# Performance work log

Measured on AMD Instinct MI355X. Metric: run time of the kernel, lower is better.

Reference implementation:

```python
import jax, jax.numpy as jnp
import numpy as np

NUM_CLASSES = 20
NUM_ANC = 5
S_ = 1 + NUM_CLASSES                   # 21
GDIM = 1 + NUM_CLASSES + 4 + 1 + 4     # 30: conf, cls20, txywh4, weight, gltrb4
ANCS_SCALE = np.array([[0.05, 0.07], [0.12, 0.15], [0.25, 0.30], [0.45, 0.55], [0.75, 0.80]], dtype=np.float32)
LOSS_W_CLS = 1.0
EPS16 = 0.0009765625  # torch.finfo(torch.float16).eps
BATCH, GRID, NBOX = 64, 38, 16
C_IN = (S_ + 4) * NUM_ANC              # 125


def ltrb2xywh(b):
    return jnp.concatenate([(b[..., :2] + b[..., 2:]) * 0.5, b[..., 2:] - b[..., :2]], -1)


def x_bce(p, g):
    p = jnp.clip(p, EPS16, 1.0 - EPS16)
    return -(g * jnp.log(p) + (1.0 - g) * jnp.log(1.0 - p))


def match_one(gboxes, glabels, ancs, grid):
    # gboxes [N,4] ltrb in [0,1]; glabels [N] in [1,NUM_CLASSES]
    xywh = ltrb2xywh(gboxes)
    cxy, wh = xywh[:, :2], xywh[:, 2:]
    # IoU between co-centered GT wh and anchor wh (both centered at origin)
    inter = jnp.minimum(wh[:, None, 0], ancs[None, :, 0]) * jnp.minimum(wh[:, None, 1], ancs[None, :, 1])
    union = (wh[:, 0] * wh[:, 1])[:, None] + (ancs[:, 0] * ancs[:, 1])[None, :] - inter
    ids_p = jnp.argmax(inter / union, axis=-1)                           # [N] best anchor per GT
    colrow = jnp.clip(jnp.floor(cxy * grid).astype(jnp.int32), 0, grid - 1)
    txy = cxy * grid - colrow.astype(cxy.dtype)                          # cell-relative offset
    twh = jnp.log(wh / ancs[ids_p])                                      # log wh ratio vs matched anchor
    weight = 2.0 - wh[:, 0] * wh[:, 1]
    onehot = jax.nn.one_hot(glabels - 1, NUM_CLASSES, dtype=gboxes.dtype)
    ones = jnp.ones((gboxes.shape[0], 1), gboxes.dtype)
    tvec = jnp.concatenate([ones, onehot, txy, twh, weight[:, None], gboxes], -1)  # [N,GDIM]
    g = jnp.zeros((grid, grid, NUM_ANC, GDIM), gboxes.dtype)
    col, row = colrow[:, 0], colrow[:, 1]
    g = g.at[row, col, :, 0].set(-1.0)       # mark all anchors at GT cell as ignore
    g = g.at[row, col, ids_p].set(tvec)      # matched anchor gets full target (conf=1)
    return g


def _loss(pyolos, gboxes_ltrb, glabels):
    batch, c, h, w = pyolos.shape
    p = pyolos.reshape(batch, S_ + 4, NUM_ANC, h * w)
    p = p.transpose(0, 3, 2, 1).reshape(batch, -1, S_ + 4)               # [B, h*w*A, 25]
    ancs = jnp.asarray(ANCS_SCALE)
    gy = jax.vmap(lambda b, l: match_one(b, l, ancs, h))(gboxes_ltrb, glabels)
    gy = gy.reshape(batch, -1, GDIM)                                     # [B, h*w*A, 30]
    gconf = gy[:, :, 0]
    mask_pos = gconf > 0
    mask_neg = gconf == 0
    nums_pos = jnp.clip(mask_pos.sum(-1).astype(jnp.float32), EPS16)
    nums_neg = jnp.clip(mask_neg.sum(-1).astype(jnp.float32), EPS16)
    mpf = mask_pos.astype(p.dtype)
    n_pos_tot = jnp.maximum(mpf.sum(), 1.0)
    # ---- cls loss over positives (masked mean == .mean() over selected) ----
    pcls = jax.nn.sigmoid(p[:, :, 1:S_])
    l_cls = (x_bce(pcls, gy[:, :, 1:S_]).sum(-1) * mpf).sum() / n_pos_tot * LOSS_W_CLS
    # ---- conf focal loss (alpha=0.5, gamma=2), replicating sum(-1).sum(-1)/nums then mean ----
    pconf = jnp.clip(jax.nn.sigmoid(p[:, :, 0]), EPS16, 1.0 - EPS16)
    l_pos = -0.5 * (1.0 - pconf) ** 2 * jnp.log(pconf) * gconf * mpf
    l_neg = -0.5 * pconf ** 2 * jnp.log(1.0 - pconf) * (1.0 - gconf) * mask_neg.astype(p.dtype)
    l_conf_pos = (l_pos.sum() / nums_pos).mean()
    l_conf_neg = (l_neg.sum() / nums_neg).mean() * 3.0
    # ---- box loss (MODE_TRAIN != 4 branch). NB: original indexes weight at S_+4+1 ----
    pxy = jax.nn.sigmoid(p[:, :, S_:S_ + 2])
    pwh = p[:, :, S_ + 2:S_ + 4]
    w_pos = gy[:, :, S_ + 4 + 1]
    l_txty = ((x_bce(pxy, gy[:, :, S_:S_ + 2]).sum(-1) * w_pos) * mpf).sum() / n_pos_tot
    l_twth = ((((pwh - gy[:, :, S_ + 2:S_ + 4]) ** 2).sum(-1) * w_pos) * mpf).sum() / n_pos_tot
    return l_conf_pos + l_conf_neg + l_cls + l_txty + l_twth


def setup_inputs():
    key = jax.random.key(0)
    k1, k2, k3, k4 = jax.random.split(key, 4)
    pyolos = jax.random.normal(k1, (BATCH, C_IN, GRID, GRID), jnp.float32)
    cxy = jax.random.uniform(k2, (BATCH, NBOX, 2), jnp.float32, 0.1, 0.9)
    wh = jax.random.uniform(k3, (BATCH, NBOX, 2), jnp.float32, 0.05, 0.3)
    gboxes_ltrb = jnp.concatenate([cxy - wh * 0.5, cxy + wh * 0.5], -1)
    glabels = jax.random.randint(k4, (BATCH, NBOX), 1, NUM_CLASSES + 1)
    return {"pyolos": pyolos, "gboxes_ltrb": gboxes_ltrb, "glabels": glabels}


def reference(pyolos, gboxes_ltrb, glabels):
    return _loss(pyolos, gboxes_ltrb, glabels)
```

## Files before the change

### kernel.cpp

```cpp
#include <hip/hip_runtime.h>

#define BATCH 64
#define GRIDW 38
#define HW 1444
#define NBOX 16
#define NANC 5
#define NCLS 20
#define SLOTS 7220
#define CIN 125
#define EPSC 0.0009765625f
#define BPB 29
#define NBLK (BATCH * BPB)
#define PSTRIDE 7

struct BoxRec {
  int   cell;
  int   ids;
  int   lab;
  float tx, ty, tw, th;
  float wleft;
};

__constant__ float ANCW[5] = {0.05f, 0.12f, 0.25f, 0.45f, 0.75f};
__constant__ float ANCH[5] = {0.07f, 0.15f, 0.30f, 0.55f, 0.80f};

__global__ void __launch_bounds__(256) main_kernel(
    const float* __restrict__ pyolos,
    const float* __restrict__ gboxes,
    const int* __restrict__ glabels,
    float* __restrict__ partials) {
  int b     = blockIdx.x / BPB;
  int chunk = blockIdx.x - b * BPB;

  __shared__ BoxRec sbox[NBOX];
  if (threadIdx.x < NBOX) {
    int n = threadIdx.x;
    const float* gb = gboxes + ((size_t)b * NBOX + n) * 4;
    float l  = gb[0], t = gb[1], r = gb[2], bt = gb[3];
    float cx = (l + r) * 0.5f, cy = (t + bt) * 0.5f;
    float w  = r - l,          h  = bt - t;
    int best = 0; float bestv = -1.0f;
    #pragma unroll
    for (int a = 0; a < NANC; ++a) {
      float inter = fminf(w, ANCW[a]) * fminf(h, ANCH[a]);
      float uni   = w * h + ANCW[a] * ANCH[a] - inter;
      float iou   = inter / uni;
      if (iou > bestv) { bestv = iou; best = a; }
    }
    int col = (int)floorf(cx * (float)GRIDW);
    int row = (int)floorf(cy * (float)GRIDW);
    col = min(max(col, 0), GRIDW - 1);
    row = min(max(row, 0), GRIDW - 1);
    BoxRec rec;
    rec.cell  = row * GRIDW + col;
    rec.ids   = best;
    rec.lab   = glabels[(size_t)b * NBOX + n] - 1;
    rec.tx    = cx * (float)GRIDW - (float)col;
    rec.ty    = cy * (float)GRIDW - (float)row;
    rec.tw    = logf(w / ANCW[best]);
    rec.th    = logf(h / ANCH[best]);
    rec.wleft = l;
    sbox[n] = rec;
  }
  __syncthreads();

  float s_pos = 0.f, s_neg = 0.f, s_cls = 0.f, s_txty = 0.f, s_twth = 0.f;
  float c_pos = 0.f, c_ign = 0.f;

  int sIdx = chunk * 256 + threadIdx.x;
  if (sIdx < SLOTS) {
    int j = sIdx / HW;
    int k = sIdx - j * HW;

    int posbox = -1; bool cellmatch = false;
    #pragma unroll
    for (int n = 0; n < NBOX; ++n) {
      if (sbox[n].cell == k) {
        cellmatch = true;
        if (sbox[n].ids == j) posbox = n;
      }
    }

    const float* pb = pyolos + (size_t)b * CIN * HW + k;
    float pconf = 1.0f / (1.0f + expf(-pb[(size_t)j * HW]));
    pconf = fminf(fmaxf(pconf, EPSC), 1.0f - EPSC);

    if (posbox >= 0) {
      c_pos = 1.f;
      float om = 1.0f - pconf;
      s_pos = -0.5f * om * om * logf(pconf);
      BoxRec rec = sbox[posbox];
      float csum = 0.f;
      for (int c = 0; c < NCLS; ++c) {
        float pc = 1.0f / (1.0f + expf(-pb[(size_t)((1 + c) * NANC + j) * HW]));
        pc = fminf(fmaxf(pc, EPSC), 1.0f - EPSC);
        csum += (c == rec.lab) ? -logf(pc) : -logf(1.0f - pc);
      }
      s_cls = csum;
      float px = 1.0f / (1.0f + expf(-pb[(size_t)(21 * NANC + j) * HW]));
      float py = 1.0f / (1.0f + expf(-pb[(size_t)(22 * NANC + j) * HW]));
      px = fminf(fmaxf(px, EPSC), 1.0f - EPSC);
      py = fminf(fmaxf(py, EPSC), 1.0f - EPSC);
      float bx = -(rec.tx * logf(px) + (1.0f - rec.tx) * logf(1.0f - px));
      float by = -(rec.ty * logf(py) + (1.0f - rec.ty) * logf(1.0f - py));
      s_txty = (bx + by) * rec.wleft;
      float pw = pb[(size_t)(23 * NANC + j) * HW];
      float ph = pb[(size_t)(24 * NANC + j) * HW];
      float dw = pw - rec.tw, dh = ph - rec.th;
      s_twth = (dw * dw + dh * dh) * rec.wleft;
    } else if (cellmatch) {
      c_ign = 1.f;
    } else {
      s_neg = -0.5f * pconf * pconf * logf(1.0f - pconf);
    }
  }

  __shared__ float red[4][PSTRIDE];
  int lane = threadIdx.x & 63;
  int wid  = threadIdx.x >> 6;
  for (int off = 32; off; off >>= 1) {
    s_pos  += __shfl_down(s_pos,  off, 64);
    s_neg  += __shfl_down(s_neg,  off, 64);
    s_cls  += __shfl_down(s_cls,  off, 64);
    s_txty += __shfl_down(s_txty, off, 64);
    s_twth += __shfl_down(s_twth, off, 64);
    c_pos  += __shfl_down(c_pos,  off, 64);
    c_ign  += __shfl_down(c_ign,  off, 64);
  }
  if (lane == 0) {
    red[wid][0] = s_pos;  red[wid][1] = s_neg; red[wid][2] = s_cls;
    red[wid][3] = s_txty; red[wid][4] = s_twth;
    red[wid][5] = c_pos;  red[wid][6] = c_ign;
  }
  __syncthreads();
  if (threadIdx.x == 0) {
    float a[PSTRIDE] = {0, 0, 0, 0, 0, 0, 0};
    for (int w2 = 0; w2 < 4; ++w2)
      for (int q = 0; q < PSTRIDE; ++q) a[q] += red[w2][q];
    float* mine = partials + (size_t)blockIdx.x * PSTRIDE;
    for (int q = 0; q < PSTRIDE; ++q) mine[q] = a[q];
  }
}

__global__ void finalize_kernel(const float* __restrict__ partials,
                                float* __restrict__ out) {
  double a[5] = {0, 0, 0, 0, 0};
  for (int i = threadIdx.x; i < NBLK; i += 256) {
    const float* p = partials + (size_t)i * PSTRIDE;
    a[0] += p[0]; a[1] += p[1]; a[2] += p[2]; a[3] += p[3]; a[4] += p[4];
  }
  __shared__ double redd[4][5];
  int lane = threadIdx.x & 63;
  int wid  = threadIdx.x >> 6;
  for (int off = 32; off; off >>= 1)
    for (int q = 0; q < 5; ++q) a[q] += __shfl_down(a[q], off, 64);
  if (lane == 0)
    for (int q = 0; q < 5; ++q) redd[wid][q] = a[q];

  double inv_pos = 0, inv_neg = 0, npos = 0;
  if (threadIdx.x < BATCH) {
    float p = 0.f, g = 0.f;
    const float* pp = partials + (size_t)threadIdx.x * BPB * PSTRIDE;
    for (int i = 0; i < BPB; ++i) { p += pp[i * PSTRIDE + 5]; g += pp[i * PSTRIDE + 6]; }
    double posf = (double)p;
    double negf = (double)SLOTS - (double)p - (double)g;
    inv_pos = 1.0 / fmax(posf, (double)EPSC);
    inv_neg = 1.0 / fmax(negf, (double)EPSC);
    npos = posf;
  }
  for (int off = 32; off; off >>= 1) {
    inv_pos += __shfl_down(inv_pos, off, 64);
    inv_neg += __shfl_down(inv_neg, off, 64);
    npos    += __shfl_down(npos,    off, 64);
  }
  __syncthreads();
  if (threadIdx.x == 0) {
    double s[5] = {0, 0, 0, 0, 0};
    for (int w2 = 0; w2 < 4; ++w2)
      for (int q = 0; q < 5; ++q) s[q] += redd[w2][q];
    double n_pos_tot = fmax(npos, 1.0);
    double loss = s[0] * (inv_pos / (double)BATCH)
                + 3.0 * s[1] * (inv_neg / (double)BATCH)
                + s[2] / n_pos_tot
                + s[3] / n_pos_tot
                + s[4] / n_pos_tot;
    out[0] = (float)loss;
  }
}

extern "C" void kernel_launch(void* const* d_in, const int* in_sizes, int n_in,
                              void* d_out, int out_size, void* d_ws, size_t ws_size,
                              hipStream_t stream) {
  const float* pyolos  = (const float*)d_in[0];
  const float* gboxes  = (const float*)d_in[1];
  const int*   glabels = (const int*)d_in[2];
  float* out = (float*)d_out;

  float* partials = (float*)d_ws;

  main_kernel<<<NBLK, 256, 0, stream>>>(pyolos, gboxes, glabels, partials);
  finalize_kernel<<<1, 256, 0, stream>>>(partials, out);
}
```

Baseline: 96.75 us.

## Fuse finalize into main kernel with one block per batch and flag-based last-block reduction

Merges the two-kernel reduce-then-finalize into a single launch. Each batch image is now handled by one block that loops over all anchor slots, writes per-batch partials including the inverse positive and negative counts, and publishes a release flag. The last block spins on the other blocks' flags and computes the final loss. This removes a kernel launch and the per-block partial scan, but cuts the grid from about 1856 blocks to 64, which lowers parallelism on a large GPU. It also relies on all blocks being co-resident and on flags that are never reset, so later calls may read stale state.

```diff
diff --git a/kernel.cpp b/kernel.cpp
--- a/kernel.cpp
+++ b/kernel.cpp
@@ -9,9 +9,8 @@
 #define SLOTS 7220
 #define CIN 125
 #define EPSC 0.0009765625f
-#define BPB 29
-#define NBLK (BATCH * BPB)
-#define PSTRIDE 7
+#define PSTRIDE 8
+#define MAGIC 0x5EEDFACEu
 
 struct BoxRec {
   int   cell;
@@ -24,13 +23,14 @@
 __constant__ float ANCW[5] = {0.05f, 0.12f, 0.25f, 0.45f, 0.75f};
 __constant__ float ANCH[5] = {0.07f, 0.15f, 0.30f, 0.55f, 0.80f};
 
-__global__ void __launch_bounds__(256) main_kernel(
+__global__ void __launch_bounds__(256) fused_kernel(
     const float* __restrict__ pyolos,
     const float* __restrict__ gboxes,
     const int* __restrict__ glabels,
-    float* __restrict__ partials) {
-  int b     = blockIdx.x / BPB;
-  int chunk = blockIdx.x - b * BPB;
+    float* __restrict__ partials,
+    unsigned int* __restrict__ flags,
+    float* __restrict__ out) {
+  int b = blockIdx.x;
 
   __shared__ BoxRec sbox[NBOX];
   if (threadIdx.x < NBOX) {
@@ -67,8 +67,8 @@
   float s_pos = 0.f, s_neg = 0.f, s_cls = 0.f, s_txty = 0.f, s_twth = 0.f;
   float c_pos = 0.f, c_ign = 0.f;
 
-  int sIdx = chunk * 256 + threadIdx.x;
-  if (sIdx < SLOTS) {
+  const float* pbase = pyolos + (size_t)b * CIN * HW;
+  for (int sIdx = threadIdx.x; sIdx < SLOTS; sIdx += 256) {
     int j = sIdx / HW;
     int k = sIdx - j * HW;
 
@@ -81,14 +81,14 @@
       }
     }
 
-    const float* pb = pyolos + (size_t)b * CIN * HW + k;
+    const float* pb = pbase + k;
     float pconf = 1.0f / (1.0f + expf(-pb[(size_t)j * HW]));
     pconf = fminf(fmaxf(pconf, EPSC), 1.0f - EPSC);
 
     if (posbox >= 0) {
-      c_pos = 1.f;
+      c_pos += 1.f;
       float om = 1.0f - pconf;
-      s_pos = -0.5f * om * om * logf(pconf);
+      s_pos += -0.5f * om * om * logf(pconf);
       BoxRec rec = sbox[posbox];
       float csum = 0.f;
       for (int c = 0; c < NCLS; ++c) {
@@ -96,26 +96,26 @@
         pc = fminf(fmaxf(pc, EPSC), 1.0f - EPSC);
         csum += (c == rec.lab) ? -logf(pc) : -logf(1.0f - pc);
       }
-      s_cls = csum;
+      s_cls += csum;
       float px = 1.0f / (1.0f + expf(-pb[(size_t)(21 * NANC + j) * HW]));
       float py = 1.0f / (1.0f + expf(-pb[(size_t)(22 * NANC + j) * HW]));
       px = fminf(fmaxf(px, EPSC), 1.0f - EPSC);
       py = fminf(fmaxf(py, EPSC), 1.0f - EPSC);
       float bx = -(rec.tx * logf(px) + (1.0f - rec.tx) * logf(1.0f - px));
       float by = -(rec.ty * logf(py) + (1.0f - rec.ty) * logf(1.0f - py));
-      s_txty = (bx + by) * rec.wleft;
+      s_txty += (bx + by) * rec.wleft;
       float pw = pb[(size_t)(23 * NANC + j) * HW];
       float ph = pb[(size_t)(24 * NANC + j) * HW];
       float dw = pw - rec.tw, dh = ph - rec.th;
-      s_twth = (dw * dw + dh * dh) * rec.wleft;
+      s_twth += (dw * dw + dh * dh) * rec.wleft;
     } else if (cellmatch) {
-      c_ign = 1.f;
+      c_ign += 1.f;
     } else {
-      s_neg = -0.5f * pconf * pconf * logf(1.0f - pconf);
-    }
-  }
-
-  __shared__ float red[4][PSTRIDE];
+      s_neg += -0.5f * pconf * pconf * logf(1.0f - pconf);
+    }
+  }
+
+  __shared__ float red[4][7];
   int lane = threadIdx.x & 63;
   int wid  = threadIdx.x >> 6;
   for (int off = 32; off; off >>= 1) {
@@ -133,58 +133,54 @@
     red[wid][5] = c_pos;  red[wid][6] = c_ign;
   }
   __syncthreads();
+
   if (threadIdx.x == 0) {
-    float a[PSTRIDE] = {0, 0, 0, 0, 0, 0, 0};
+    float a[7] = {0, 0, 0, 0, 0, 0, 0};
     for (int w2 = 0; w2 < 4; ++w2)
-      for (int q = 0; q < PSTRIDE; ++q) a[q] += red[w2][q];
-    float* mine = partials + (size_t)blockIdx.x * PSTRIDE;
-    for (int q = 0; q < PSTRIDE; ++q) mine[q] = a[q];
-  }
-}
-
-__global__ void finalize_kernel(const float* __restrict__ partials,
-                                float* __restrict__ out) {
-  double a[5] = {0, 0, 0, 0, 0};
-  for (int i = threadIdx.x; i < NBLK; i += 256) {
-    const float* p = partials + (size_t)i * PSTRIDE;
-    a[0] += p[0]; a[1] += p[1]; a[2] += p[2]; a[3] += p[3]; a[4] += p[4];
-  }
-  __shared__ double redd[4][5];
-  int lane = threadIdx.x & 63;
-  int wid  = threadIdx.x >> 6;
-  for (int off = 32; off; off >>= 1)
-    for (int q = 0; q < 5; ++q) a[q] += __shfl_down(a[q], off, 64);
-  if (lane == 0)
-    for (int q = 0; q < 5; ++q) redd[wid][q] = a[q];
-
-  double inv_pos = 0, inv_neg = 0, npos = 0;
-  if (threadIdx.x < BATCH) {
-    float p = 0.f, g = 0.f;
-    const float* pp = partials + (size_t)threadIdx.x * BPB * PSTRIDE;
-    for (int i = 0; i < BPB; ++i) { p += pp[i * PSTRIDE + 5]; g += pp[i * PSTRIDE + 6]; }
-    double posf = (double)p;
-    double negf = (double)SLOTS - (double)p - (double)g;
-    inv_pos = 1.0 / fmax(posf, (double)EPSC);
-    inv_neg = 1.0 / fmax(negf, (double)EPSC);
-    npos = posf;
-  }
-  for (int off = 32; off; off >>= 1) {
-    inv_pos += __shfl_down(inv_pos, off, 64);
-    inv_neg += __shfl_down(inv_neg, off, 64);
-    npos    += __shfl_down(npos,    off, 64);
-  }
-  __syncthreads();
-  if (threadIdx.x == 0) {
-    double s[5] = {0, 0, 0, 0, 0};
-    for (int w2 = 0; w2 < 4; ++w2)
-      for (int q = 0; q < 5; ++q) s[q] += redd[w2][q];
-    double n_pos_tot = fmax(npos, 1.0);
-    double loss = s[0] * (inv_pos / (double)BATCH)
-                + 3.0 * s[1] * (inv_neg / (double)BATCH)
-                + s[2] / n_pos_tot
-                + s[3] / n_pos_tot
-                + s[4] / n_pos_tot;
-    out[0] = (float)loss;
+      for (int q = 0; q < 7; ++q) a[q] += red[w2][q];
+    float npos = a[5];
+    float nneg = (float)SLOTS - a[5] - a[6];
+    float* mine = partials + (size_t)b * PSTRIDE;
+    mine[0] = a[0];
+    mine[1] = a[1];
+    mine[2] = a[2];
+    mine[3] = a[3];
+    mine[4] = a[4];
+    mine[5] = 1.0f / fmaxf(npos, EPSC);
+    mine[6] = 1.0f / fmaxf(nneg, EPSC);
+    mine[7] = npos;
+    __threadfence();
+    __hip_atomic_store(&flags[b], MAGIC, __ATOMIC_RELEASE, __HIP_MEMORY_SCOPE_AGENT);
+
+    if (b == BATCH - 1) {
+      for (int i = 0; i < BATCH; ++i) {
+        while (__hip_atomic_load(&flags[i], __ATOMIC_ACQUIRE,
+                                 __HIP_MEMORY_SCOPE_AGENT) != MAGIC) {
+          __builtin_amdgcn_s_sleep(1);
+        }
+      }
+      __threadfence();
+      double spos = 0, sneg = 0, scls = 0, stxty = 0, stwth = 0;
+      double sinvp = 0, sinvn = 0, snpos = 0;
+      for (int i = 0; i < BATCH; ++i) {
+        const float* p = partials + (size_t)i * PSTRIDE;
+        spos  += (double)__hip_atomic_load(&p[0], __ATOMIC_RELAXED, __HIP_MEMORY_SCOPE_AGENT);
+        sneg  += (double)__hip_atomic_load(&p[1], __ATOMIC_RELAXED, __HIP_MEMORY_SCOPE_AGENT);
+        scls  += (double)__hip_atomic_load(&p[2], __ATOMIC_RELAXED, __HIP_MEMORY_SCOPE_AGENT);
+        stxty += (double)__hip_atomic_load(&p[3], __ATOMIC_RELAXED, __HIP_MEMORY_SCOPE_AGENT);
+        stwth += (double)__hip_atomic_load(&p[4], __ATOMIC_RELAXED, __HIP_MEMORY_SCOPE_AGENT);
+        sinvp += (double)__hip_atomic_load(&p[5], __ATOMIC_RELAXED, __HIP_MEMORY_SCOPE_AGENT);
+        sinvn += (double)__hip_atomic_load(&p[6], __ATOMIC_RELAXED, __HIP_MEMORY_SCOPE_AGENT);
+        snpos += (double)__hip_atomic_load(&p[7], __ATOMIC_RELAXED, __HIP_MEMORY_SCOPE_AGENT);
+      }
+      double n_pos_tot = fmax(snpos, 1.0);
+      double loss = spos * (sinvp / (double)BATCH)
+                  + 3.0 * sneg * (sinvn / (double)BATCH)
+                  + scls  / n_pos_tot
+                  + stxty / n_pos_tot
+                  + stwth / n_pos_tot;
+      out[0] = (float)loss;
+    }
   }
 }
 
@@ -196,8 +192,9 @@
   const int*   glabels = (const int*)d_in[2];
   float* out = (float*)d_out;
 
-  float* partials = (float*)d_ws;
-
-  main_kernel<<<NBLK, 256, 0, stream>>>(pyolos, gboxes, glabels, partials);
-  finalize_kernel<<<1, 256, 0, stream>>>(partials, out);
+  float*        partials = (float*)d_ws;
+  unsigned int* flags    = (unsigned int*)((char*)d_ws + 2048);
+
+  fused_kernel<<<BATCH, 256, 0, stream>>>(pyolos, gboxes, glabels,
+                                          partials, flags, out);
 }
```

Result: slower. 137.0 us (+41.6%).
